# Optimization experiments

Measured on AMD Instinct MI355X. Metric: run time of the kernel, lower is better.

Reference implementation:

```python
import jax, jax.numpy as jnp
import numpy as np

N_NODES = 100000
N_EDGES = 1600000
D_IN = 128
D_HID = 64


def _linear_params(key, d_in, d_out, bias=True):
    k1, k2 = jax.random.split(key)
    bound = 1.0 / np.sqrt(d_in)
    W = jax.random.uniform(k1, (d_out, d_in), jnp.float32, -bound, bound)
    if bias:
        b = jax.random.uniform(k2, (d_out,), jnp.float32, -bound, bound)
        return W, b
    return W


def setup_inputs() -> dict:
    key = jax.random.key(0)
    ks = jax.random.split(key, 12)
    x = jax.random.normal(ks[0], (N_NODES, D_IN), jnp.float32)
    edge_index = jax.random.randint(ks[1], (2, N_EDGES), 0, N_NODES, dtype=jnp.int64)
    # SAGEConv layer 1 (D_IN -> D_HID): lin_l (bias), lin_r (no bias)
    Wl1, bl1 = _linear_params(ks[2], D_IN, D_HID)
    Wr1 = _linear_params(ks[3], D_IN, D_HID, bias=False)
    # SAGEConv layer 2 (D_HID -> D_HID)
    Wl2, bl2 = _linear_params(ks[4], D_HID, D_HID)
    Wr2 = _linear_params(ks[5], D_HID, D_HID, bias=False)
    # SAGEConv layer 3 (conv2, single layer, D_HID -> D_HID)
    Wl3, bl3 = _linear_params(ks[6], D_HID, D_HID)
    Wr3 = _linear_params(ks[7], D_HID, D_HID, bias=False)
    # classifier (D_HID -> 1)
    Wc, bc = _linear_params(ks[8], D_HID, 1)
    return {
        "x": x, "edge_index": edge_index,
        "Wl1": Wl1, "bl1": bl1, "Wr1": Wr1,
        "Wl2": Wl2, "bl2": bl2, "Wr2": Wr2,
        "Wl3": Wl3, "bl3": bl3, "Wr3": Wr3,
        "Wc": Wc, "bc": bc,
    }


def _sage_conv(x, src, dst, deg_inv, Wl, bl, Wr):
    # mean-aggregate neighbor features: gather on src, scatter-sum to dst
    msg = x[src]  # [E, d] -- dominant memory traffic
    agg = jax.ops.segment_sum(msg, dst, num_segments=N_NODES) * deg_inv  # [N, d]
    return agg @ Wl.T + bl + x @ Wr.T


def reference(x, edge_index, Wl1, bl1, Wr1, Wl2, bl2, Wr2, Wl3, bl3, Wr3, Wc, bc):
    src, dst = edge_index[0], edge_index[1]
    deg = jax.ops.segment_sum(jnp.ones((src.shape[0],), x.dtype), dst, num_segments=N_NODES)
    deg_inv = (1.0 / jnp.maximum(deg, 1.0))[:, None]  # [N, 1]
    # conv1 = GraphSAGE(num_layers=2): sage -> relu -> sage
    h = _sage_conv(x, src, dst, deg_inv, Wl1, bl1, Wr1)
    h = jax.nn.relu(h)
    h = _sage_conv(h, src, dst, deg_inv, Wl2, bl2, Wr2)
    # outer relu
    h = jax.nn.relu(h)
    # conv2 = GraphSAGE(num_layers=1): single sage
    h = _sage_conv(h, src, dst, deg_inv, Wl3, bl3, Wr3)
    h = jax.nn.relu(h)
    out = h @ Wc.T + bc  # [N, 1]
    return out.squeeze()  # [N]
```

## Files before the change

kernel.cpp:

```cpp
#include <hip/hip_runtime.h>
#include <hip/hip_bf16.h>


__global__ __launch_bounds__(256) void count_deg_slot(const int* __restrict__ dst,
                                                      int* __restrict__ deg,
                                                      int* __restrict__ eslot, int nE) {
    int e = blockIdx.x * 256 + threadIdx.x;
    if (e < nE) eslot[e] = atomicAdd(&deg[dst[e]], 1);
}

__global__ __launch_bounds__(256) void scan_partial(const int* __restrict__ deg,
                                                    int* __restrict__ partial, int n) {
    __shared__ int red[256];
    int base = blockIdx.x * 2048;
    int t = threadIdx.x;
    int sum = 0;
    for (int j = 0; j < 8; ++j) {
        int i = base + t + 256 * j;
        if (i < n) sum += deg[i];
    }
    red[t] = sum;
    __syncthreads();
    for (int o = 128; o; o >>= 1) {
        if (t < o) red[t] += red[t + o];
        __syncthreads();
    }
    if (t == 0) partial[blockIdx.x] = red[0];
}

__global__ __launch_bounds__(256) void scan_block(int* __restrict__ partial, int B) {
    __shared__ int tmp[256];
    int t = threadIdx.x;
    int orig = (t < B) ? partial[t] : 0;
    tmp[t] = orig;
    __syncthreads();
    for (int o = 1; o < 256; o <<= 1) {
        int v = (t >= o) ? tmp[t - o] : 0;
        __syncthreads();
        tmp[t] += v;
        __syncthreads();
    }
    if (t < B) partial[t] = tmp[t] - orig;
}

__global__ __launch_bounds__(256) void scan_final(const int* __restrict__ deg,
                                                  const int* __restrict__ partial,
                                                  int* __restrict__ off,
                                                  float* __restrict__ deg_inv, int n) {
    __shared__ int lds[2048];
    __shared__ int tsum[256];
    int base = blockIdx.x * 2048;
    int t = threadIdx.x;
    for (int j = 0; j < 8; ++j) {
        int i = base + t + 256 * j;
        lds[t + 256 * j] = (i < n) ? deg[i] : 0;
    }
    __syncthreads();
    int loc[8];
    int s0 = 0;
    for (int j = 0; j < 8; ++j) {
        loc[j] = s0;
        s0 += lds[t * 8 + j];
    }
    int orig = s0;
    tsum[t] = s0;
    __syncthreads();
    for (int o = 1; o < 256; o <<= 1) {
        int v = (t >= o) ? tsum[t - o] : 0;
        __syncthreads();
        tsum[t] += v;
        __syncthreads();
    }
    int tpre = tsum[t] - orig + partial[blockIdx.x];
    for (int j = 0; j < 8; ++j) {
        int i = base + t * 8 + j;
        if (i < n) {
            int d = lds[t * 8 + j];
            int ex = tpre + loc[j];
            off[i] = ex;
            deg_inv[i] = 1.0f / (float)((d > 1) ? d : 1);
            if (i == n - 1) off[n] = ex + d;
        }
    }
}

__global__ __launch_bounds__(256) void fill_csr(const int* __restrict__ src,
                                                const int* __restrict__ dst,
                                                const int* __restrict__ off,
                                                const int* __restrict__ eslot,
                                                int* __restrict__ csr, int nE) {
    int e = blockIdx.x * 256 + threadIdx.x;
    if (e >= nE) return;
    csr[off[dst[e]] + eslot[e]] = src[e];
}

template <int K>
__global__ __launch_bounds__(256) void gemm_dual(const float* __restrict__ X,
                                                 const float* __restrict__ Wl,
                                                 const float* __restrict__ Wr,
                                                 const float* __restrict__ bl,
                                                 float* __restrict__ Y,
                                                 float* __restrict__ S, int nNodes) {
    __shared__ float wl_s[64][K + 1];
    __shared__ float wr_s[64][K + 1];
    __shared__ float4 x_s[16][K / 4];
    int t = threadIdx.x;
    for (int i = t; i < 64 * K; i += 256) {
        int f = i / K, k = i % K;
        wl_s[f][k] = Wl[i];
        wr_s[f][k] = Wr[i];
    }
    const int f = t & 63, s = t >> 6;
    __syncthreads();
    const float blf = bl[f];
    const float4* Xv = reinterpret_cast<const float4*>(X);
    const float4 z4 = make_float4(0.f, 0.f, 0.f, 0.f);

    for (int tile = blockIdx.x * 16; tile < nNodes; tile += gridDim.x * 16) {
        __syncthreads();
        for (int i = t; i < 16 * (K / 4); i += 256) {
            int r = i / (K / 4), kq = i % (K / 4);
            int row = tile + r;
            x_s[r][kq] = (row < nNodes) ? Xv[(size_t)row * (K / 4) + kq] : z4;
        }
        __syncthreads();
        float accY[4] = {0.f, 0.f, 0.f, 0.f};
        float accS[4] = {0.f, 0.f, 0.f, 0.f};
#pragma unroll 4
        for (int kq = 0; kq < K / 4; ++kq) {
            const int k0 = kq * 4;
            float wl0 = wl_s[f][k0 + 0], wl1 = wl_s[f][k0 + 1];
            float wl2 = wl_s[f][k0 + 2], wl3 = wl_s[f][k0 + 3];
            float wr0 = wr_s[f][k0 + 0], wr1 = wr_s[f][k0 + 1];
            float wr2 = wr_s[f][k0 + 2], wr3 = wr_s[f][k0 + 3];
#pragma unroll
            for (int j = 0; j < 4; ++j) {
                float4 xv = x_s[s + 4 * j][kq];
                accY[j] = fmaf(xv.x, wl0, accY[j]);
                accY[j] = fmaf(xv.y, wl1, accY[j]);
                accY[j] = fmaf(xv.z, wl2, accY[j]);
                accY[j] = fmaf(xv.w, wl3, accY[j]);
                accS[j] = fmaf(xv.x, wr0, accS[j]);
                accS[j] = fmaf(xv.y, wr1, accS[j]);
                accS[j] = fmaf(xv.z, wr2, accS[j]);
                accS[j] = fmaf(xv.w, wr3, accS[j]);
            }
        }
#pragma unroll
        for (int j = 0; j < 4; ++j) {
            int row = tile + s + 4 * j;
            if (row < nNodes) {
                Y[(size_t)row * 64 + f] = accY[j];
                S[(size_t)row * 64 + f] = accS[j] + blf;
            }
        }
    }
}

__device__ __forceinline__ float4 agg_core(const float4* __restrict__ Yv,
                                           const int* __restrict__ csr,
                                           int e0, int e1, int lane) {
    const int q = lane >> 4;
    const int fq = lane & 15;
    float4 acc = make_float4(0.f, 0.f, 0.f, 0.f);
    for (int base = e0; base < e1; base += 64) {
        int cnt = min(64, e1 - base);
        int mysrc = (lane < cnt) ? csr[base + lane] : 0;
        int nFull = cnt >> 2;
        int j = 0;
        for (; j + 4 <= nFull; j += 4) {
            int s0 = __shfl(mysrc, 4 * j + q);
            int s1 = __shfl(mysrc, 4 * j + 4 + q);
            int s2 = __shfl(mysrc, 4 * j + 8 + q);
            int s3 = __shfl(mysrc, 4 * j + 12 + q);
            float4 v0 = Yv[(size_t)s0 * 16 + fq];
            float4 v1 = Yv[(size_t)s1 * 16 + fq];
            float4 v2 = Yv[(size_t)s2 * 16 + fq];
            float4 v3 = Yv[(size_t)s3 * 16 + fq];
            acc.x += v0.x; acc.y += v0.y; acc.z += v0.z; acc.w += v0.w;
            acc.x += v1.x; acc.y += v1.y; acc.z += v1.z; acc.w += v1.w;
            acc.x += v2.x; acc.y += v2.y; acc.z += v2.z; acc.w += v2.w;
            acc.x += v3.x; acc.y += v3.y; acc.z += v3.z; acc.w += v3.w;
        }
        if (j + 2 <= nFull) {
            int s0 = __shfl(mysrc, 4 * j + q);
            int s1 = __shfl(mysrc, 4 * j + 4 + q);
            float4 v0 = Yv[(size_t)s0 * 16 + fq];
            float4 v1 = Yv[(size_t)s1 * 16 + fq];
            acc.x += v0.x; acc.y += v0.y; acc.z += v0.z; acc.w += v0.w;
            acc.x += v1.x; acc.y += v1.y; acc.z += v1.z; acc.w += v1.w;
            j += 2;
        }
        if (j < nFull) {
            int sj = __shfl(mysrc, 4 * j + q);
            float4 v = Yv[(size_t)sj * 16 + fq];
            acc.x += v.x; acc.y += v.y; acc.z += v.z; acc.w += v.w;
        }
        int rem = cnt & 3;
        if (rem) {
            int sj = __shfl(mysrc, 4 * nFull + q);
            if (q < rem) {
                float4 v = Yv[(size_t)sj * 16 + fq];
                acc.x += v.x; acc.y += v.y; acc.z += v.z; acc.w += v.w;
            }
        }
    }
    acc.x += __shfl_xor(acc.x, 16); acc.y += __shfl_xor(acc.y, 16);
    acc.z += __shfl_xor(acc.z, 16); acc.w += __shfl_xor(acc.w, 16);
    acc.x += __shfl_xor(acc.x, 32); acc.y += __shfl_xor(acc.y, 32);
    acc.z += __shfl_xor(acc.z, 32); acc.w += __shfl_xor(acc.w, 32);
    return acc;
}

__global__ __launch_bounds__(256) void agg_relu(const float* __restrict__ Y,
                                                const float* __restrict__ S,
                                                const int* __restrict__ csr,
                                                const int* __restrict__ off,
                                                const float* __restrict__ deg_inv,
                                                float* __restrict__ H, int nNodes) {
    int wave = threadIdx.x >> 6;
    int lane = threadIdx.x & 63;
    int n = blockIdx.x * 4 + wave;
    if (n >= nNodes) return;
    int e0 = off[n], e1 = off[n + 1];
    float di = deg_inv[n];
    float4 sv = ((const float4*)S)[(size_t)n * 16 + (lane & 15)];
    float4 acc = agg_core((const float4*)Y, csr, e0, e1, lane);
    if (lane < 16) {
        float4 h;
        h.x = fmaxf(fmaf(acc.x, di, sv.x), 0.f);
        h.y = fmaxf(fmaf(acc.y, di, sv.y), 0.f);
        h.z = fmaxf(fmaf(acc.z, di, sv.z), 0.f);
        h.w = fmaxf(fmaf(acc.w, di, sv.w), 0.f);
        ((float4*)H)[(size_t)n * 16 + lane] = h;
    }
}

__global__ __launch_bounds__(256) void agg_classify(const float* __restrict__ Y,
                                                    const float* __restrict__ S,
                                                    const int* __restrict__ csr,
                                                    const int* __restrict__ off,
                                                    const float* __restrict__ deg_inv,
                                                    const float* __restrict__ Wc,
                                                    const float* __restrict__ bc,
                                                    float* __restrict__ out, int nNodes) {
    int wave = threadIdx.x >> 6;
    int lane = threadIdx.x & 63;
    int n = blockIdx.x * 4 + wave;
    if (n >= nNodes) return;
    int e0 = off[n], e1 = off[n + 1];
    float di = deg_inv[n];
    float4 sv = ((const float4*)S)[(size_t)n * 16 + (lane & 15)];
    float4 wc = ((const float4*)Wc)[lane & 15];
    float bias = bc[0];
    float4 acc = agg_core((const float4*)Y, csr, e0, e1, lane);
    if (lane < 16) {
        float hx = fmaxf(fmaf(acc.x, di, sv.x), 0.f);
        float hy = fmaxf(fmaf(acc.y, di, sv.y), 0.f);
        float hz = fmaxf(fmaf(acc.z, di, sv.z), 0.f);
        float hw = fmaxf(fmaf(acc.w, di, sv.w), 0.f);
        float c = hx * wc.x + hy * wc.y + hz * wc.z + hw * wc.w;
#pragma unroll
        for (int o = 8; o; o >>= 1) c += __shfl_xor(c, o);
        if (lane == 0) out[n] = c + bias;
    }
}

extern "C" void kernel_launch(void* const* d_in, const int* in_sizes, int n_in,
                              void* d_out, int out_size, void* d_ws, size_t ws_size,
                              hipStream_t stream) {
    const float* x   = (const float*)d_in[0];
    const int*   ei  = (const int*)d_in[1];
    const float* Wl1 = (const float*)d_in[2];
    const float* bl1 = (const float*)d_in[3];
    const float* Wr1 = (const float*)d_in[4];
    const float* Wl2 = (const float*)d_in[5];
    const float* bl2 = (const float*)d_in[6];
    const float* Wr2 = (const float*)d_in[7];
    const float* Wl3 = (const float*)d_in[8];
    const float* bl3 = (const float*)d_in[9];
    const float* Wr3 = (const float*)d_in[10];
    const float* Wc  = (const float*)d_in[11];
    const float* bc  = (const float*)d_in[12];
    float* out = (float*)d_out;

    const int N = in_sizes[0] / 128;
    const int E = in_sizes[1] / 2;
    const int* src = ei;
    const int* dst = ei + E;

    char* p = (char*)d_ws;
    auto alloc = [&](size_t bytes) -> void* {
        char* r = p;
        p += (bytes + 255) & ~(size_t)255;
        return (void*)r;
    };
    int*   deg     = (int*)alloc((size_t)N * 4);
    int*   off     = (int*)alloc((size_t)(N + 1) * 4);
    int*   eslot   = (int*)alloc((size_t)E * 4);
    int*   partial = (int*)alloc(256 * 4);
    int*   csr     = (int*)alloc((size_t)E * 4);
    float* deg_inv = (float*)alloc((size_t)N * 4);
    float* y       = (float*)alloc((size_t)N * 64 * 4);
    float* s       = (float*)alloc((size_t)N * 64 * 4);
    float* h       = (float*)alloc((size_t)N * 64 * 4);

    hipMemsetAsync(deg, 0, (size_t)N * 4, stream);

    const int B = (N + 2047) / 2048;

    count_deg_slot<<<(E + 255) / 256, 256, 0, stream>>>(dst, deg, eslot, E);
    scan_partial<<<B, 256, 0, stream>>>(deg, partial, N);
    scan_block<<<1, 256, 0, stream>>>(partial, B);
    scan_final<<<B, 256, 0, stream>>>(deg, partial, off, deg_inv, N);
    fill_csr<<<(E + 255) / 256, 256, 0, stream>>>(src, dst, off, eslot, csr, E);

    int aggGrid = (N + 3) / 4;

    gemm_dual<128><<<2048, 256, 0, stream>>>(x, Wl1, Wr1, bl1, y, s, N);
    agg_relu<<<aggGrid, 256, 0, stream>>>(y, s, csr, off, deg_inv, h, N);
    gemm_dual<64><<<2048, 256, 0, stream>>>(h, Wl2, Wr2, bl2, y, s, N);
    agg_relu<<<aggGrid, 256, 0, stream>>>(y, s, csr, off, deg_inv, h, N);
    gemm_dual<64><<<2048, 256, 0, stream>>>(h, Wl3, Wr3, bl3, y, s, N);
    agg_classify<<<aggGrid, 256, 0, stream>>>(y, s, csr, off, deg_inv, Wc, bc, out, N);
}
```

Baseline: 540.8 us.

## Load GEMM input rows directly into registers with 8-row tiles per thread

The dense dual-GEMM kernel no longer stages X tiles in shared memory behind barriers. Each thread now loads float4 slices of its 8 rows straight from global memory and accumulates 8 rows by 2 outputs, in 512-thread blocks covering 64-row tiles on a smaller grid. This removes the per-tile syncthreads and LDS traffic for X and doubles per-thread row reuse of the weights. In exchange, the 64 threads sharing a row each issue redundant global/L1 loads of it, and register pressure rises.

```diff
diff --git a/kernel.cpp b/kernel.cpp
--- a/kernel.cpp
+++ b/kernel.cpp
@@ -95,63 +95,74 @@
 }
 
 template <int K>
-__global__ __launch_bounds__(256) void gemm_dual(const float* __restrict__ X,
-                                                 const float* __restrict__ Wl,
-                                                 const float* __restrict__ Wr,
-                                                 const float* __restrict__ bl,
-                                                 float* __restrict__ Y,
-                                                 float* __restrict__ S, int nNodes) {
+__global__ __launch_bounds__(512, 4) void gemm_dual(const float* __restrict__ X,
+                                                    const float* __restrict__ Wl,
+                                                    const float* __restrict__ Wr,
+                                                    const float* __restrict__ bl,
+                                                    float* __restrict__ Y,
+                                                    float* __restrict__ S, int nNodes) {
     __shared__ float wl_s[64][K + 1];
     __shared__ float wr_s[64][K + 1];
-    __shared__ float4 x_s[16][K / 4];
-    int t = threadIdx.x;
-    for (int i = t; i < 64 * K; i += 256) {
+    const int t = threadIdx.x;
+    for (int i = t; i < 64 * K; i += 512) {
         int f = i / K, k = i % K;
         wl_s[f][k] = Wl[i];
         wr_s[f][k] = Wr[i];
     }
-    const int f = t & 63, s = t >> 6;
+    const int f = t & 63;
+    const int s = t >> 6;
     __syncthreads();
     const float blf = bl[f];
-    const float4* Xv = reinterpret_cast<const float4*>(X);
-    const float4 z4 = make_float4(0.f, 0.f, 0.f, 0.f);
-
-    for (int tile = blockIdx.x * 16; tile < nNodes; tile += gridDim.x * 16) {
-        __syncthreads();
-        for (int i = t; i < 16 * (K / 4); i += 256) {
-            int r = i / (K / 4), kq = i % (K / 4);
-            int row = tile + r;
-            x_s[r][kq] = (row < nNodes) ? Xv[(size_t)row * (K / 4) + kq] : z4;
-        }
-        __syncthreads();
-        float accY[4] = {0.f, 0.f, 0.f, 0.f};
-        float accS[4] = {0.f, 0.f, 0.f, 0.f};
-#pragma unroll 4
-        for (int kq = 0; kq < K / 4; ++kq) {
-            const int k0 = kq * 4;
+    const float4* __restrict__ Xv = reinterpret_cast<const float4*>(X);
+    constexpr int KQ = K / 4;
+    const int nTiles = (nNodes + 63) >> 6;
+
+    for (int tb = blockIdx.x; tb < nTiles; tb += gridDim.x) {
+        const int r0 = tb * 64 + s * 8;
+        size_t xb[8];
+#pragma unroll
+        for (int j = 0; j < 8; ++j) {
+            int rc = r0 + j;
+            rc = (rc < nNodes) ? rc : (nNodes - 1);
+            xb[j] = (size_t)rc * KQ;
+        }
+        float accY[8] = {0.f, 0.f, 0.f, 0.f, 0.f, 0.f, 0.f, 0.f};
+        float accS[8] = {0.f, 0.f, 0.f, 0.f, 0.f, 0.f, 0.f, 0.f};
+#pragma unroll 2
+        for (int kq = 0; kq < KQ; ++kq) {
+            float4 xr[8];
+#pragma unroll
+            for (int j = 0; j < 8; ++j) xr[j] = Xv[xb[j] + kq];
+            const int k0 = 4 * kq;
             float wl0 = wl_s[f][k0 + 0], wl1 = wl_s[f][k0 + 1];
             float wl2 = wl_s[f][k0 + 2], wl3 = wl_s[f][k0 + 3];
             float wr0 = wr_s[f][k0 + 0], wr1 = wr_s[f][k0 + 1];
             float wr2 = wr_s[f][k0 + 2], wr3 = wr_s[f][k0 + 3];
 #pragma unroll
-            for (int j = 0; j < 4; ++j) {
-                float4 xv = x_s[s + 4 * j][kq];
-                accY[j] = fmaf(xv.x, wl0, accY[j]);
-                accY[j] = fmaf(xv.y, wl1, accY[j]);
-                accY[j] = fmaf(xv.z, wl2, accY[j]);
-                accY[j] = fmaf(xv.w, wl3, accY[j]);
-                accS[j] = fmaf(xv.x, wr0, accS[j]);
-                accS[j] = fmaf(xv.y, wr1, accS[j]);
-                accS[j] = fmaf(xv.z, wr2, accS[j]);
-                accS[j] = fmaf(xv.w, wr3, accS[j]);
+            for (int j = 0; j < 8; ++j) {
+                accY[j] = fmaf(xr[j].x, wl0, accY[j]);
+                accY[j] = fmaf(xr[j].y, wl1, accY[j]);
+                accY[j] = fmaf(xr[j].z, wl2, accY[j]);
+                accY[j] = fmaf(xr[j].w, wl3, accY[j]);
+                accS[j] = fmaf(xr[j].x, wr0, accS[j]);
+                accS[j] = fmaf(xr[j].y, wr1, accS[j]);
+                accS[j] = fmaf(xr[j].z, wr2, accS[j]);
+                accS[j] = fmaf(xr[j].w, wr3, accS[j]);
             }
         }
-#pragma unroll
-        for (int j = 0; j < 4; ++j) {
-            int row = tile + s + 4 * j;
-            if (row < nNodes) {
-                Y[(size_t)row * 64 + f] = accY[j];
-                S[(size_t)row * 64 + f] = accS[j] + blf;
+        if (r0 + 7 < nNodes) {
+#pragma unroll
+            for (int j = 0; j < 8; ++j) {
+                Y[(size_t)(r0 + j) * 64 + f] = accY[j];
+                S[(size_t)(r0 + j) * 64 + f] = accS[j] + blf;
+            }
+        } else {
+#pragma unroll
+            for (int j = 0; j < 8; ++j) {
+                if (r0 + j < nNodes) {
+                    Y[(size_t)(r0 + j) * 64 + f] = accY[j];
+                    S[(size_t)(r0 + j) * 64 + f] = accS[j] + blf;
+                }
             }
         }
     }
@@ -317,10 +328,10 @@
 
     int aggGrid = (N + 3) / 4;
 
-    gemm_dual<128><<<2048, 256, 0, stream>>>(x, Wl1, Wr1, bl1, y, s, N);
+    gemm_dual<128><<<512, 512, 0, stream>>>(x, Wl1, Wr1, bl1, y, s, N);
     agg_relu<<<aggGrid, 256, 0, stream>>>(y, s, csr, off, deg_inv, h, N);
-    gemm_dual<64><<<2048, 256, 0, stream>>>(h, Wl2, Wr2, bl2, y, s, N);
+    gemm_dual<64><<<512, 512, 0, stream>>>(h, Wl2, Wr2, bl2, y, s, N);
     agg_relu<<<aggGrid, 256, 0, stream>>>(y, s, csr, off, deg_inv, h, N);
-    gemm_dual<64><<<2048, 256, 0, stream>>>(h, Wl3, Wr3, bl3, y, s, N);
+    gemm_dual<64><<<512, 512, 0, stream>>>(h, Wl3, Wr3, bl3, y, s, N);
     agg_classify<<<aggGrid, 256, 0, stream>>>(y, s, csr, off, deg_inv, Wc, bc, out, N);
 }
```

Result: slower. 620.0 us (+14.7%).

## Retile dual GEMM to 64-row tiles with swizzled float4 weight layout

Applied to the files above, without the earlier changes.

Reworks the per-layer dual GEMM so each 512-thread block processes 64 rows per tile, with each thread computing two output features for four rows. Weights are stored as float4 in shared memory with an XOR swizzle so threads reading different feature rows avoid bank conflicts. Edge rows are clamped instead of zero-filled, and outputs are written as float2. This raises arithmetic reuse per shared load and cuts per-tile sync overhead, at the cost of higher register use and different grid sizes.

```diff
diff --git a/kernel.cpp b/kernel.cpp
--- a/kernel.cpp
+++ b/kernel.cpp
@@ -95,63 +95,91 @@
 }
 
 template <int K>
-__global__ __launch_bounds__(256) void gemm_dual(const float* __restrict__ X,
-                                                 const float* __restrict__ Wl,
-                                                 const float* __restrict__ Wr,
-                                                 const float* __restrict__ bl,
-                                                 float* __restrict__ Y,
-                                                 float* __restrict__ S, int nNodes) {
-    __shared__ float wl_s[64][K + 1];
-    __shared__ float wr_s[64][K + 1];
-    __shared__ float4 x_s[16][K / 4];
-    int t = threadIdx.x;
-    for (int i = t; i < 64 * K; i += 256) {
-        int f = i / K, k = i % K;
-        wl_s[f][k] = Wl[i];
-        wr_s[f][k] = Wr[i];
-    }
-    const int f = t & 63, s = t >> 6;
-    __syncthreads();
-    const float blf = bl[f];
-    const float4* Xv = reinterpret_cast<const float4*>(X);
-    const float4 z4 = make_float4(0.f, 0.f, 0.f, 0.f);
-
-    for (int tile = blockIdx.x * 16; tile < nNodes; tile += gridDim.x * 16) {
-        __syncthreads();
-        for (int i = t; i < 16 * (K / 4); i += 256) {
-            int r = i / (K / 4), kq = i % (K / 4);
+__global__ __launch_bounds__(512, 4) void gemm_dual(const float* __restrict__ X,
+                                                    const float* __restrict__ Wl,
+                                                    const float* __restrict__ Wr,
+                                                    const float* __restrict__ bl,
+                                                    float* __restrict__ Y,
+                                                    float* __restrict__ S, int nNodes) {
+    constexpr int QPR = K / 4;
+    __shared__ float4 wl_s[64 * QPR];
+    __shared__ float4 wr_s[64 * QPR];
+    __shared__ float4 x_s[64 * QPR];
+    const int t = threadIdx.x;
+
+    const float4* __restrict__ Wl4 = reinterpret_cast<const float4*>(Wl);
+    const float4* __restrict__ Wr4 = reinterpret_cast<const float4*>(Wr);
+    for (int i = t; i < 64 * QPR; i += 512) {
+        int f = i / QPR, q = i % QPR;
+        int qs = q ^ ((f >> 1) & (QPR - 1));
+        wl_s[f * QPR + qs] = Wl4[i];
+        wr_s[f * QPR + qs] = Wr4[i];
+    }
+
+    const int p = t & 31;
+    const int s = t >> 5;
+    const int fe0 = 2 * p;
+    const int pm = p & (QPR - 1);
+    const float2 blv = reinterpret_cast<const float2*>(bl)[p];
+    const float4* __restrict__ Xv = reinterpret_cast<const float4*>(X);
+    const float4* __restrict__ wlA = wl_s + (size_t)fe0 * QPR;
+    const float4* __restrict__ wlB = wl_s + (size_t)(fe0 + 1) * QPR;
+    const float4* __restrict__ wrA = wr_s + (size_t)fe0 * QPR;
+    const float4* __restrict__ wrB = wr_s + (size_t)(fe0 + 1) * QPR;
+
+    for (int tile = blockIdx.x * 64; tile < nNodes; tile += gridDim.x * 64) {
+        __syncthreads();
+        for (int i = t; i < 64 * QPR; i += 512) {
+            int r = i / QPR, q = i % QPR;
             int row = tile + r;
-            x_s[r][kq] = (row < nNodes) ? Xv[(size_t)row * (K / 4) + kq] : z4;
-        }
-        __syncthreads();
-        float accY[4] = {0.f, 0.f, 0.f, 0.f};
-        float accS[4] = {0.f, 0.f, 0.f, 0.f};
-#pragma unroll 4
-        for (int kq = 0; kq < K / 4; ++kq) {
-            const int k0 = kq * 4;
-            float wl0 = wl_s[f][k0 + 0], wl1 = wl_s[f][k0 + 1];
-            float wl2 = wl_s[f][k0 + 2], wl3 = wl_s[f][k0 + 3];
-            float wr0 = wr_s[f][k0 + 0], wr1 = wr_s[f][k0 + 1];
-            float wr2 = wr_s[f][k0 + 2], wr3 = wr_s[f][k0 + 3];
+            row = (row < nNodes) ? row : (nNodes - 1);
+            x_s[i] = Xv[(size_t)row * QPR + q];
+        }
+        __syncthreads();
+
+        float2 accY[4], accS[4];
+#pragma unroll
+        for (int j = 0; j < 4; ++j) {
+            accY[j] = make_float2(0.f, 0.f);
+            accS[j] = make_float2(0.f, 0.f);
+        }
+#pragma unroll 2
+        for (int kq = 0; kq < QPR; ++kq) {
+            const int qs = kq ^ pm;
+            float4 wl0 = wlA[qs];
+            float4 wl1 = wlB[qs];
+            float4 wr0 = wrA[qs];
+            float4 wr1 = wrB[qs];
 #pragma unroll
             for (int j = 0; j < 4; ++j) {
-                float4 xv = x_s[s + 4 * j][kq];
-                accY[j] = fmaf(xv.x, wl0, accY[j]);
-                accY[j] = fmaf(xv.y, wl1, accY[j]);
-                accY[j] = fmaf(xv.z, wl2, accY[j]);
-                accY[j] = fmaf(xv.w, wl3, accY[j]);
-                accS[j] = fmaf(xv.x, wr0, accS[j]);
-                accS[j] = fmaf(xv.y, wr1, accS[j]);
-                accS[j] = fmaf(xv.z, wr2, accS[j]);
-                accS[j] = fmaf(xv.w, wr3, accS[j]);
+                float4 xv = x_s[(s * 4 + j) * QPR + kq];
+                accY[j].x = fmaf(xv.x, wl0.x, accY[j].x);
+                accY[j].x = fmaf(xv.y, wl0.y, accY[j].x);
+                accY[j].x = fmaf(xv.z, wl0.z, accY[j].x);
+                accY[j].x = fmaf(xv.w, wl0.w, accY[j].x);
+                accY[j].y = fmaf(xv.x, wl1.x, accY[j].y);
+                accY[j].y = fmaf(xv.y, wl1.y, accY[j].y);
+                accY[j].y = fmaf(xv.z, wl1.z, accY[j].y);
+                accY[j].y = fmaf(xv.w, wl1.w, accY[j].y);
+                accS[j].x = fmaf(xv.x, wr0.x, accS[j].x);
+                accS[j].x = fmaf(xv.y, wr0.y, accS[j].x);
+                accS[j].x = fmaf(xv.z, wr0.z, accS[j].x);
+                accS[j].x = fmaf(xv.w, wr0.w, accS[j].x);
+                accS[j].y = fmaf(xv.x, wr1.x, accS[j].y);
+                accS[j].y = fmaf(xv.y, wr1.y, accS[j].y);
+                accS[j].y = fmaf(xv.z, wr1.z, accS[j].y);
+                accS[j].y = fmaf(xv.w, wr1.w, accS[j].y);
             }
         }
+
+        const int r0 = tile + s * 4;
 #pragma unroll
         for (int j = 0; j < 4; ++j) {
-            int row = tile + s + 4 * j;
+            int row = r0 + j;
             if (row < nNodes) {
-                Y[(size_t)row * 64 + f] = accY[j];
-                S[(size_t)row * 64 + f] = accS[j] + blf;
+                reinterpret_cast<float2*>(Y + (size_t)row * 64)[p] = accY[j];
+                reinterpret_cast<float2*>(S + (size_t)row * 64)[p] =
+                    make_float2(accS[j].x + blv.x, accS[j].y + blv.y);
             }
         }
     }
@@ -317,10 +345,10 @@
 
     int aggGrid = (N + 3) / 4;
 
-    gemm_dual<128><<<2048, 256, 0, stream>>>(x, Wl1, Wr1, bl1, y, s, N);
+    gemm_dual<128><<<512, 512, 0, stream>>>(x, Wl1, Wr1, bl1, y, s, N);
     agg_relu<<<aggGrid, 256, 0, stream>>>(y, s, csr, off, deg_inv, h, N);
-    gemm_dual<64><<<2048, 256, 0, stream>>>(h, Wl2, Wr2, bl2, y, s, N);
+    gemm_dual<64><<<768, 512, 0, stream>>>(h, Wl2, Wr2, bl2, y, s, N);
     agg_relu<<<aggGrid, 256, 0, stream>>>(y, s, csr, off, deg_inv, h, N);
-    gemm_dual<64><<<2048, 256, 0, stream>>>(h, Wl3, Wr3, bl3, y, s, N);
+    gemm_dual<64><<<768, 512, 0, stream>>>(h, Wl3, Wr3, bl3, y, s, N);
     agg_classify<<<aggGrid, 256, 0, stream>>>(y, s, csr, off, deg_inv, Wc, bc, out, N);
 }
```

New measurement: 507.5 us. 6.2% less time.
